# Performance work log

Measured on AMD Instinct MI355X. Metric: run time of the kernel, lower is better.

The kernel has to match this reference:

```python
import jax, jax.numpy as jnp
import numpy as np

Hr, Wr = 64, 2048          # range-view size
Hb, Wb = 512, 512          # BEV size
R_MAX = 50.0
VERT_ROW = Hr // 2         # vert_row default in __init__
B, C = 4, 64
TWO_PI = 2.0 * np.pi


def _sample_coords():
    """Replicates the buffer math in RV2BEV.__init__ + grid_sample's
    align_corners=True unnormalization. Returns flat px (N=Hb*Wb,) and scalar py."""
    yy, xx = np.meshgrid(np.arange(Hb), np.arange(Wb), indexing='ij')
    y = (yy - Hb / 2 + 0.5) * R_MAX / (Hb / 2 - 0.5)
    x = (xx - Wb / 2 + 0.5) * R_MAX / (Wb / 2 - 0.5)
    phi = (np.arctan2(y, x) + TWO_PI) % TWO_PI
    col = Wr - 1 - phi / TWO_PI * (Wr - 1)
    gx = col / Wr * 2 - 1                 # normalized grid x in [-1,1)
    gy = VERT_ROW / Hr * 2 - 1            # normalized grid y (scalar)
    px = (gx + 1) / 2 * (Wr - 1)          # align_corners=True pixel coords
    py = (gy + 1) / 2 * (Hr - 1)
    return px.reshape(-1).astype(np.float32), np.float32(py)

_PX, _PY = _sample_coords()


def _grid_sample_row(rv_feat, px, py):
    """Bilinear grid_sample for a grid whose y-coordinate is a single constant
    row. All coords are in-bounds by construction, so zero-padding never fires."""
    x0 = jnp.floor(px).astype(jnp.int32)
    x1 = jnp.clip(x0 + 1, 0, Wr - 1)
    y0 = int(np.floor(py))
    y1 = min(y0 + 1, Hr - 1)
    wx = (px - x0.astype(px.dtype)).astype(rv_feat.dtype)     # (N,)
    wy = jnp.asarray(py - y0, dtype=rv_feat.dtype)            # scalar
    # interpolate the two relevant RV rows first: (B,C,Wr)
    row = rv_feat[:, :, y0, :] * (1 - wy) + rv_feat[:, :, y1, :] * wy
    # gather along azimuth: (B,C,N)
    s0 = row[:, :, x0]
    s1 = row[:, :, x1]
    return s0 * (1 - wx) + s1 * wx


def setup_inputs() -> dict:
    key = jax.random.key(0)
    k1, k2 = jax.random.split(key)
    rv_feat = jax.random.normal(k1, (B, C, Hr, Wr), dtype=jnp.float32)
    ref_bev = jax.random.normal(k2, (B, C, Hb, Wb), dtype=jnp.float32)
    return {"rv_feat": rv_feat, "ref_bev": ref_bev}


def reference(rv_feat, ref_bev):
    # The torch forward clones ref_bev then overwrites EVERY (b, y, x) index
    # via the scatter (oidx covers all positions of the first B batches), so
    # the result is exactly the sampled features reshaped to the BEV grid.
    sampled = _grid_sample_row(rv_feat, jnp.asarray(_PX), _PY)   # (B,C,N)
    bev = sampled.reshape(rv_feat.shape[0], rv_feat.shape[1], Hb, Wb)
    return bev
```

## Files before the change

### kernel.cpp

```cpp
#include <hip/hip_runtime.h>
#include <math.h>

constexpr int Hr = 64;
constexpr int Wr = 2048;
constexpr int Hb = 512;
constexpr int Wb = 512;
constexpr int B  = 4;
constexpr int C  = 64;
constexpr int BC = B * C;
constexpr int NPIX = Hb * Wb;

constexpr int T   = 16384;
constexpr int NT  = NPIX / T;
constexpr int TPB = 128;

typedef float f32x4 __attribute__((ext_vector_type(4)));


__global__ __launch_bounds__(256) void prep_px(float* __restrict__ pxbuf)
{
    const int n  = blockIdx.x * 256 + threadIdx.x;
    const float cs = 50.0f / 255.5f;
    const float c1 = 2047.0f / 6.28318530717958647692f;
    const float c2 = 2047.0f / 2048.0f;
    const float y = ((float)(n >> 9)  - 255.5f) * cs;
    const float x = ((float)(n & 511) - 255.5f) * cs;
    float phi = atan2f(y, x);
    phi = (phi < 0.0f) ? phi + 6.28318530717958647692f : phi;
    pxbuf[n] = (2047.0f - phi * c1) * c2;
}

__global__ __launch_bounds__(TPB) void sample_kernel(
    const float* __restrict__ rv,
    const float* __restrict__ pxbuf,
    float* __restrict__ out)
{
    __shared__ float row[Wr];

    const int tile = blockIdx.x;
    const int ch   = blockIdx.y;
    const int tid  = threadIdx.x;

    {
        const float* chb = rv + (size_t)ch * (Hr * Wr) + (size_t)31 * Wr;
        const f32x4* r31 = (const f32x4*)chb;
        const f32x4* r32 = (const f32x4*)(chb + Wr);
        f32x4* dst = (f32x4*)row;
        #pragma unroll
        for (int q = 0; q < 4; ++q) {
            const int i = tid + q * TPB;
            dst[i] = r31[i] * 0.5f + r32[i] * 0.5f;
        }
    }
    __syncthreads();

    const f32x4* px4  = (const f32x4*)(pxbuf + (size_t)tile * T);
    f32x4*       out4 = (f32x4*)(out + (size_t)ch * NPIX + (size_t)tile * T);

    #pragma unroll 4
    for (int k = 0; k < T / 4 / TPB; ++k) {
        const int i = k * TPB + tid;
        const f32x4 p = px4[i];
        f32x4 r;
        #pragma unroll
        for (int j = 0; j < 4; ++j) {
            const int   xi = (int)p[j];
            const float w  = p[j] - (float)xi;
            r[j] = row[xi] * (1.0f - w) + row[xi + 1] * w;
        }
        __builtin_nontemporal_store(r, out4 + i);
    }
}

extern "C" void kernel_launch(void* const* d_in, const int* in_sizes, int n_in,
                              void* d_out, int out_size, void* d_ws, size_t ws_size,
                              hipStream_t stream) {
    const float* rv_feat = (const float*)d_in[0];
    float* out = (float*)d_out;
    float* pxbuf = (float*)d_ws;

    prep_px<<<dim3(NPIX / 256), dim3(256), 0, stream>>>(pxbuf);
    sample_kernel<<<dim3(NT, BC), dim3(TPB), 0, stream>>>(rv_feat, pxbuf, out);
}
```

Baseline: 62.85 us.

## Precompute integer index and weight, use fewer larger sampling blocks

The prep kernel now stores the integer azimuth index and fractional weight as separate vectorized buffers, so the sampling loop no longer does a float-to-int conversion. The lerp becomes a single FMA form. The sampling grid shrinks from 16 tiles per channel with 128 threads to 2 halves per channel with 512 threads. This cuts the redundant per-block row loads and syncs. In exchange, each iteration reads twice as much coordinate data (8 MB vs 4 MB per channel pass, mostly L2-resident), and the grid drops to 512 blocks, which may hurt latency hiding.

```diff
diff --git a/kernel.cpp b/kernel.cpp
--- a/kernel.cpp
+++ b/kernel.cpp
@@ -10,34 +10,48 @@
 constexpr int BC = B * C;
 constexpr int NPIX = Hb * Wb;
 
-constexpr int T   = 16384;
-constexpr int NT  = NPIX / T;
-constexpr int TPB = 128;
+constexpr int TPB  = 512;
+constexpr int HALF = NPIX / 2;
+constexpr int NIT  = HALF / 4 / TPB;
 
 typedef float f32x4 __attribute__((ext_vector_type(4)));
+typedef int   i32x4 __attribute__((ext_vector_type(4)));
 
 
-__global__ __launch_bounds__(256) void prep_px(float* __restrict__ pxbuf)
+__global__ __launch_bounds__(256) void prep_px(
+    i32x4* __restrict__ xig,
+    f32x4* __restrict__ wg)
 {
-    const int n  = blockIdx.x * 256 + threadIdx.x;
+    const int g  = blockIdx.x * 256 + threadIdx.x;
     const float cs = 50.0f / 255.5f;
     const float c1 = 2047.0f / 6.28318530717958647692f;
     const float c2 = 2047.0f / 2048.0f;
-    const float y = ((float)(n >> 9)  - 255.5f) * cs;
-    const float x = ((float)(n & 511) - 255.5f) * cs;
-    float phi = atan2f(y, x);
-    phi = (phi < 0.0f) ? phi + 6.28318530717958647692f : phi;
-    pxbuf[n] = (2047.0f - phi * c1) * c2;
+    i32x4 xo; f32x4 wo;
+    #pragma unroll
+    for (int j = 0; j < 4; ++j) {
+        const int n = g * 4 + j;
+        const float y = ((float)(n >> 9)  - 255.5f) * cs;
+        const float x = ((float)(n & 511) - 255.5f) * cs;
+        float phi = atan2f(y, x);
+        phi = (phi < 0.0f) ? phi + 6.28318530717958647692f : phi;
+        const float px = (2047.0f - phi * c1) * c2;
+        const int   xi = (int)px;
+        xo[j] = xi;
+        wo[j] = px - (float)xi;
+    }
+    xig[g] = xo;
+    wg[g]  = wo;
 }
 
 __global__ __launch_bounds__(TPB) void sample_kernel(
     const float* __restrict__ rv,
-    const float* __restrict__ pxbuf,
+    const i32x4* __restrict__ xig,
+    const f32x4* __restrict__ wg,
     float* __restrict__ out)
 {
     __shared__ float row[Wr];
 
-    const int tile = blockIdx.x;
+    const int half = blockIdx.x;
     const int ch   = blockIdx.y;
     const int tid  = threadIdx.x;
 
@@ -45,28 +59,26 @@
         const float* chb = rv + (size_t)ch * (Hr * Wr) + (size_t)31 * Wr;
         const f32x4* r31 = (const f32x4*)chb;
         const f32x4* r32 = (const f32x4*)(chb + Wr);
-        f32x4* dst = (f32x4*)row;
-        #pragma unroll
-        for (int q = 0; q < 4; ++q) {
-            const int i = tid + q * TPB;
-            dst[i] = r31[i] * 0.5f + r32[i] * 0.5f;
-        }
+        ((f32x4*)row)[tid] = r31[tid] * 0.5f + r32[tid] * 0.5f;
     }
     __syncthreads();
 
-    const f32x4* px4  = (const f32x4*)(pxbuf + (size_t)tile * T);
-    f32x4*       out4 = (f32x4*)(out + (size_t)ch * NPIX + (size_t)tile * T);
+    const size_t g0 = (size_t)half * (HALF / 4);
+    const i32x4* xs   = xig + g0;
+    const f32x4* ws   = wg  + g0;
+    f32x4*       out4 = (f32x4*)(out + (size_t)ch * NPIX) + g0;
 
     #pragma unroll 4
-    for (int k = 0; k < T / 4 / TPB; ++k) {
+    for (int k = 0; k < NIT; ++k) {
         const int i = k * TPB + tid;
-        const f32x4 p = px4[i];
+        const i32x4 xv = xs[i];
+        const f32x4 wv = ws[i];
         f32x4 r;
         #pragma unroll
         for (int j = 0; j < 4; ++j) {
-            const int   xi = (int)p[j];
-            const float w  = p[j] - (float)xi;
-            r[j] = row[xi] * (1.0f - w) + row[xi + 1] * w;
+            const float a = row[xv[j]];
+            const float b = row[xv[j] + 1];
+            r[j] = a + wv[j] * (b - a);
         }
         __builtin_nontemporal_store(r, out4 + i);
     }
@@ -77,8 +89,10 @@
                               hipStream_t stream) {
     const float* rv_feat = (const float*)d_in[0];
     float* out = (float*)d_out;
-    float* pxbuf = (float*)d_ws;
 
-    prep_px<<<dim3(NPIX / 256), dim3(256), 0, stream>>>(pxbuf);
-    sample_kernel<<<dim3(NT, BC), dim3(TPB), 0, stream>>>(rv_feat, pxbuf, out);
+    i32x4* xig = (i32x4*)d_ws;
+    f32x4* wg  = (f32x4*)((char*)d_ws + NPIX * 4);
+
+    prep_px<<<dim3(NPIX / 4 / 256), dim3(256), 0, stream>>>(xig, wg);
+    sample_kernel<<<dim3(2, BC), dim3(TPB), 0, stream>>>(rv_feat, xig, wg, out);
 }
```

Result: faster. 60.91 us (-3.1%).
